# Performance work log

Hardware: AMD Instinct MI355X
Metric: run time of the kernel (lower is better)

Reference implementation:

```python
import jax, jax.numpy as jnp
import numpy as np

N_NODES = 50000
N_EDGES = 800000
N_GRAPHS = 64
IN_CH = 128
HID_CH = 128
FC_CH = 128


def setup_inputs() -> dict:
    key = jax.random.key(0)
    ks = jax.random.split(key, 12)

    def lin_w(k, fan_in, fan_out):
        return jax.random.normal(k, (fan_in, fan_out), jnp.float32) * (1.0 / np.sqrt(fan_in))

    return {
        "x": jax.random.normal(ks[0], (N_NODES, IN_CH), jnp.float32),
        "edge_index": jax.random.randint(ks[1], (2, N_EDGES), 0, N_NODES, dtype=jnp.int64),
        "batch_vec": jnp.sort(jax.random.randint(ks[2], (N_NODES,), 0, N_GRAPHS, dtype=jnp.int64)),
        "W1": lin_w(ks[3], IN_CH, HID_CH),
        "b1": jnp.zeros((HID_CH,), jnp.float32),
        "W2": lin_w(ks[4], HID_CH, HID_CH),
        "b2": jnp.zeros((HID_CH,), jnp.float32),
        "W3": lin_w(ks[5], HID_CH, FC_CH),
        "b3": jnp.zeros((FC_CH,), jnp.float32),
        "fcW1": lin_w(ks[6], FC_CH, IN_CH),
        "fcb1": jnp.zeros((IN_CH,), jnp.float32),
        "fcW2": lin_w(ks[7], IN_CH, 2),
        "fcb2": jnp.zeros((2,), jnp.float32),
    }


def reference(x, edge_index, batch_vec, W1, b1, W2, b2, W3, b3, fcW1, fcb1, fcW2, fcb2):
    n = x.shape[0]
    row, col = edge_index[0], edge_index[1]  # src -> dst

    # GCN symmetric normalization with self-loops: deg[j] = in-degree(j) + 1
    deg = jnp.zeros((n,), x.dtype).at[col].add(1.0) + 1.0
    inv_sqrt = jax.lax.rsqrt(deg)
    edge_norm = inv_sqrt[row] * inv_sqrt[col]  # [E]
    self_norm = (inv_sqrt * inv_sqrt)[:, None]  # [N,1], self-loop weight 1/deg

    def gcn(h, W, b):
        h = h @ W  # [N, out]
        agg = jnp.zeros_like(h).at[col].add(h[row] * edge_norm[:, None])
        return agg + h * self_norm + b

    h = jax.nn.relu(gcn(x, W1, b1))
    h = jax.nn.relu(gcn(h, W2, b2))
    h = jax.nn.relu(gcn(h, W3, b3))
    h = jax.nn.relu(h @ fcW1 + fcb1)
    h = h @ fcW2 + fcb2  # [N, 2]

    # global mean pool per graph
    sums = jax.ops.segment_sum(h, batch_vec, num_segments=N_GRAPHS)
    cnts = jax.ops.segment_sum(jnp.ones((n,), h.dtype), batch_vec, num_segments=N_GRAPHS)
    pooled = sums / jnp.maximum(cnts, 1.0)[:, None]  # [G, 2]
    return jax.nn.softmax(pooled, axis=1)
```

## Files before the change

kernel.cpp:

```cpp
#include <hip/hip_runtime.h>


#define CH 128
#define BSH 7
#define SEG 4096
#define EPW 4096
#define SAF 136
#define SC8 144

typedef unsigned short ushortT;
typedef unsigned int uintT;
typedef unsigned char ucharT;
typedef __attribute__((ext_vector_type(8))) short short8;
typedef __attribute__((ext_vector_type(4))) float floatx4;
typedef __attribute__((ext_vector_type(2))) float floatx2;

__device__ __forceinline__ float bf2f(uintT u) {
    return __uint_as_float(u << 16);
}
__device__ __forceinline__ ushortT f2bf(float f) {
    uintT x = __float_as_uint(f);
    return (ushortT)((x + 0x7fffu + ((x >> 16) & 1u)) >> 16);
}
__device__ __forceinline__ void dec4(uintT u, float* o) {
    floatx2 lo = __builtin_amdgcn_cvt_pk_f32_fp8((int)u, false);
    floatx2 hi = __builtin_amdgcn_cvt_pk_f32_fp8((int)u, true);
    o[0] = lo.x; o[1] = lo.y; o[2] = hi.x; o[3] = hi.y;
}
__device__ __forceinline__ void dec16(uint4 v, float* o) {
    dec4(v.x, o); dec4(v.y, o + 4); dec4(v.z, o + 8); dec4(v.w, o + 12);
}

__global__ __launch_bounds__(256) void k_bin(const int* __restrict__ row,
                                             const int* __restrict__ col,
                                             int* __restrict__ bfill,
                                             uintT* __restrict__ seg,
                                             const float* __restrict__ X,
                                             ucharT* __restrict__ Xb,
                                             const float* __restrict__ w0,
                                             const float* __restrict__ w1,
                                             const float* __restrict__ w2,
                                             const float* __restrict__ w3,
                                             ushortT* __restrict__ Whi,
                                             int E, int NBB, int NB, int total4) {
    __shared__ uintT staged[EPW];
    __shared__ int target[EPW];
    __shared__ int sval[512];
    __shared__ int horig[512];
    __shared__ int pcnt[512];
    __shared__ int gbase[512];
    const int t = threadIdx.x;

    if ((int)blockIdx.x >= NBB) {
        if ((int)blockIdx.x < NBB + 256) {
            int idx = ((int)blockIdx.x - NBB) * 256 + t;
            int m = idx >> 14;
            int r2 = idx & 16383;
            int n = r2 >> 7;
            int k = r2 & 127;
            const float* W = (m == 0) ? w0 : (m == 1) ? w1 : (m == 2) ? w2 : w3;
            Whi[m * 16384 + n * CH + k] = f2bf(W[k * CH + n]);
        } else {
            int i = ((int)blockIdx.x - NBB - 256) * 256 + t;
            if (i < total4) {
                float4 v = reinterpret_cast<const float4*>(X)[i];
                int r0 = __builtin_amdgcn_cvt_pk_fp8_f32(v.x, v.y, 0, false);
                int r1 = __builtin_amdgcn_cvt_pk_fp8_f32(v.z, v.w, r0, true);
                reinterpret_cast<int*>(Xb)[i] = r1;
            }
        }
        return;
    }

    const int e0 = blockIdx.x * EPW;
    const int cnt = min(EPW, E - e0);

    sval[t] = 0; sval[t + 256] = 0;
    __syncthreads();

    int er[16], ec[16];
#pragma unroll
    for (int i = 0; i < 16; ++i) {
        int le = i * 256 + t;
        if (le < cnt) {
            er[i] = row[e0 + le];
            ec[i] = col[e0 + le];
            atomicAdd(&sval[ec[i] >> BSH], 1);
        }
    }
    __syncthreads();
    horig[t] = sval[t]; horig[t + 256] = sval[t + 256];
    __syncthreads();
    for (int off = 1; off < 512; off <<= 1) {
        int a = (t >= off) ? sval[t - off] : 0;
        int b2 = sval[t + 256 - off];
        __syncthreads();
        sval[t] += a;
        sval[t + 256] += b2;
        __syncthreads();
    }
    for (int b = t; b < 512; b += 256) {
        int h = horig[b];
        pcnt[b] = sval[b] - h;
        gbase[b] = (h > 0 && b < NB) ? atomicAdd(&bfill[b], h) : 0;
    }
    __syncthreads();
#pragma unroll
    for (int i = 0; i < 16; ++i) {
        int le = i * 256 + t;
        if (le < cnt) {
            int b = ec[i] >> BSH;
            int j = atomicAdd(&pcnt[b], 1);
            staged[j] = (uintT)er[i] | ((uintT)ec[i] << 16);
            int lo = sval[b] - horig[b];
            target[j] = b * SEG + gbase[b] + (j - lo);
        }
    }
    __syncthreads();
    for (int s = t; s < cnt; s += 256) seg[target[s]] = staged[s];
}

__global__ __launch_bounds__(512) void k_binvs_bscan(const int* __restrict__ bfill,
                                                     const uintT* __restrict__ seg,
                                                     float* __restrict__ invs,
                                                     int* __restrict__ bbase,
                                                     int* __restrict__ indptr,
                                                     float* __restrict__ sums,
                                                     float* __restrict__ cnts,
                                                     int* __restrict__ tdone,
                                                     int NB, int N, int E, int G) {
    const int b = blockIdx.x;
    const int t = threadIdx.x;
    if (b < NB) {
        __shared__ int h[128];
        if (t < 128) h[t] = 0;
        __syncthreads();
        int cnt = bfill[b];
        const uintT* sp = seg + (size_t)b * SEG;
        for (int s = t; s < cnt; s += 512) atomicAdd(&h[(sp[s] >> 16) & 127], 1);
        __syncthreads();
        int d = b * 128 + t;
        if (t < 128 && d < N) invs[d] = rsqrtf((float)h[t] + 1.0f);
    } else {
        __shared__ int s[512];
        for (int i = t; i < 3 * G; i += 512) {
            if (i < 2 * G) sums[i] = 0.f;
            else cnts[i - 2 * G] = 0.f;
        }
        if (t == 0) atomicExch(tdone, 0);
        int v = (t < NB) ? bfill[t] : 0;
        s[t] = v;
        __syncthreads();
        for (int off = 1; off < 512; off <<= 1) {
            int a = (t >= off) ? s[t - off] : 0;
            __syncthreads();
            s[t] += a;
            __syncthreads();
        }
        if (t < NB) bbase[t] = s[t] - v;
        if (t == 0) indptr[N] = E;
    }
}

__global__ __launch_bounds__(256) void k_scatter(const int* __restrict__ bfill,
                                                 const int* __restrict__ bbase,
                                                 const uintT* __restrict__ seg,
                                                 const float* __restrict__ invs,
                                                 int* __restrict__ indptr,
                                                 uintT* __restrict__ epack,
                                                 int N) {
    __shared__ uintT staged[SEG];
    __shared__ int h[128];
    __shared__ int sc[128];
    __shared__ int pc[128];
    const int t = threadIdx.x;
    const int b = blockIdx.x;
    const int cnt = bfill[b];
    const int base = bbase[b];
    const uintT* sp = seg + (size_t)b * SEG;

    if (t < 128) h[t] = 0;
    __syncthreads();
    for (int s = t; s < cnt; s += 256) atomicAdd(&h[(sp[s] >> 16) & 127], 1);
    __syncthreads();
    if (t < 128) sc[t] = h[t];
    __syncthreads();
    for (int off = 1; off < 128; off <<= 1) {
        int a = (t >= off && t < 128) ? sc[t - off] : 0;
        __syncthreads();
        if (t < 128) sc[t] += a;
        __syncthreads();
    }
    if (t < 128) {
        int excl = sc[t] - h[t];
        pc[t] = excl;
        int d = b * 128 + t;
        if (d < N) indptr[d] = base + excl;
    }
    __syncthreads();
    for (int s = t; s < cnt; s += 256) {
        uintT rc = sp[s];
        int src = (int)(rc & 0xffffu), dst = (int)(rc >> 16);
        int j = atomicAdd(&pc[dst & 127], 1);
        float nrm = invs[src] * invs[dst];
        staged[j] = (uintT)src | ((uintT)f2bf(nrm) << 16);
    }
    __syncthreads();
    for (int s = t; s < cnt; s += 256) epack[base + s] = staged[s];
}

__global__ __launch_bounds__(256) void k_agg(const ucharT* __restrict__ H8,
                                             const uintT* __restrict__ epack,
                                             const int* __restrict__ indptr,
                                             const float* __restrict__ invs,
                                             ucharT* __restrict__ Z8, int N) {
    const int wave = threadIdx.x >> 6, lane = threadIdx.x & 63;
    const int ng = lane >> 3;
    const int l = lane & 7;
    const int node = blockIdx.x * 32 + wave * 8 + ng;
    if (node >= N) return;

    const uint4* H4 = reinterpret_cast<const uint4*>(H8);

    float acc[16];
    {
        float sn = invs[node];
        float sn2 = sn * sn;
        float d[16];
        dec16(H4[(size_t)node * 8 + l], d);
#pragma unroll
        for (int j = 0; j < 16; ++j) acc[j] = sn2 * d[j];
    }

    int p = indptr[node];
    int p1 = indptr[node + 1];

    if (p + 8 <= p1) {
        uintT e0[8];
#pragma unroll
        for (int i = 0; i < 8; ++i) e0[i] = epack[p + i];
        for (; p + 16 <= p1; p += 8) {
            uintT e1[8];
#pragma unroll
            for (int i = 0; i < 8; ++i) e1[i] = epack[p + 8 + i];
            uint4 g[8];
#pragma unroll
            for (int i = 0; i < 8; ++i) g[i] = H4[(size_t)(int)(e0[i] & 0xffffu) * 8 + l];
#pragma unroll
            for (int i = 0; i < 8; ++i) {
                float wv = bf2f(e0[i] >> 16);
                float d[16];
                dec16(g[i], d);
#pragma unroll
                for (int j = 0; j < 16; ++j) acc[j] += wv * d[j];
            }
#pragma unroll
            for (int i = 0; i < 8; ++i) e0[i] = e1[i];
        }
        {
            uint4 g[8];
#pragma unroll
            for (int i = 0; i < 8; ++i) g[i] = H4[(size_t)(int)(e0[i] & 0xffffu) * 8 + l];
#pragma unroll
            for (int i = 0; i < 8; ++i) {
                float wv = bf2f(e0[i] >> 16);
                float d[16];
                dec16(g[i], d);
#pragma unroll
                for (int j = 0; j < 16; ++j) acc[j] += wv * d[j];
            }
            p += 8;
        }
    }
    int rem = p1 - p;
    if (rem > 0) {
        uintT e[8];
#pragma unroll
        for (int i = 0; i < 8; ++i) e[i] = epack[(i < rem) ? p + i : p];
        uint4 g[8];
#pragma unroll
        for (int i = 0; i < 8; ++i) g[i] = H4[(size_t)(int)(e[i] & 0xffffu) * 8 + l];
#pragma unroll
        for (int i = 0; i < 8; ++i) {
            float wv = (i < rem) ? bf2f(e[i] >> 16) : 0.f;
            float d[16];
            dec16(g[i], d);
#pragma unroll
            for (int j = 0; j < 16; ++j) acc[j] += wv * d[j];
        }
    }

    uint4 o;
    {
        int r0 = __builtin_amdgcn_cvt_pk_fp8_f32(acc[0], acc[1], 0, false);
        r0 = __builtin_amdgcn_cvt_pk_fp8_f32(acc[2], acc[3], r0, true);
        int r1 = __builtin_amdgcn_cvt_pk_fp8_f32(acc[4], acc[5], 0, false);
        r1 = __builtin_amdgcn_cvt_pk_fp8_f32(acc[6], acc[7], r1, true);
        int r2 = __builtin_amdgcn_cvt_pk_fp8_f32(acc[8], acc[9], 0, false);
        r2 = __builtin_amdgcn_cvt_pk_fp8_f32(acc[10], acc[11], r2, true);
        int r3 = __builtin_amdgcn_cvt_pk_fp8_f32(acc[12], acc[13], 0, false);
        r3 = __builtin_amdgcn_cvt_pk_fp8_f32(acc[14], acc[15], r3, true);
        o.x = (uintT)r0; o.y = (uintT)r1; o.z = (uintT)r2; o.w = (uintT)r3;
    }
    reinterpret_cast<uint4*>(Z8)[(size_t)node * 8 + l] = o;
}

__global__ __launch_bounds__(256) void k_gemm(const ucharT* __restrict__ In8,
                                              const ushortT* __restrict__ Whi,
                                              const float* __restrict__ Bias,
                                              ucharT* __restrict__ Out8, int N) {
    __shared__ ushortT As[128 * SAF];
    __shared__ ushortT Ws[128 * SAF];

    const int tid = threadIdx.x;
    const int wave = tid >> 6, lane = tid & 63;
    const int quad = lane >> 4, l15 = lane & 15;
    const int mBase = (wave >> 1) * 64, nBase = (wave & 1) * 64;
    const int row0 = blockIdx.x * 128;
    const int r = tid >> 1, half = tid & 1;

    {
        int grow = row0 + r;
        uint4 a8 = {0, 0, 0, 0}, b8 = {0, 0, 0, 0}, c8 = {0, 0, 0, 0}, d8v = {0, 0, 0, 0};
        if (grow < N) {
            const uint4* s = reinterpret_cast<const uint4*>(In8 + (size_t)grow * CH + half * 64);
            a8 = s[0]; b8 = s[1]; c8 = s[2]; d8v = s[3];
        }
        uintT wds[16] = {a8.x, a8.y, a8.z, a8.w, b8.x, b8.y, b8.z, b8.w,
                         c8.x, c8.y, c8.z, c8.w, d8v.x, d8v.y, d8v.z, d8v.w};
#pragma unroll
        for (int q = 0; q < 16; ++q) {
            float d[4];
            dec4(wds[q], d);
            uint2 o;
            o.x = (uintT)f2bf(d[0]) | ((uintT)f2bf(d[1]) << 16);
            o.y = (uintT)f2bf(d[2]) | ((uintT)f2bf(d[3]) << 16);
            *reinterpret_cast<uint2*>(&As[r * SAF + half * 64 + q * 4]) = o;
        }
        const uint4* sh = reinterpret_cast<const uint4*>(Whi + r * CH + half * 64);
#pragma unroll
        for (int q = 0; q < 8; ++q)
            *reinterpret_cast<uint4*>(&Ws[r * SAF + half * 64 + q * 8]) = sh[q];
    }
    __syncthreads();

    floatx4 acc[4][4];
    const floatx4 zero4 = {0.f, 0.f, 0.f, 0.f};
#pragma unroll
    for (int i = 0; i < 4; i++)
#pragma unroll
        for (int j = 0; j < 4; j++) acc[i][j] = zero4;

#pragma unroll
    for (int ks = 0; ks < 4; ++ks) {
        short8 af[4], wf[4];
#pragma unroll
        for (int mt = 0; mt < 4; ++mt)
            af[mt] = *reinterpret_cast<const short8*>(&As[(mBase + mt * 16 + l15) * SAF + ks * 32 + quad * 8]);
#pragma unroll
        for (int nt = 0; nt < 4; ++nt)
            wf[nt] = *reinterpret_cast<const short8*>(&Ws[(nBase + nt * 16 + l15) * SAF + ks * 32 + quad * 8]);
#pragma unroll
        for (int mt = 0; mt < 4; ++mt)
#pragma unroll
            for (int nt = 0; nt < 4; ++nt)
                acc[mt][nt] = __builtin_amdgcn_mfma_f32_16x16x32_bf16(af[mt], wf[nt], acc[mt][nt], 0, 0, 0);
    }
    __syncthreads();

    float bb[4];
#pragma unroll
    for (int nt = 0; nt < 4; ++nt) bb[nt] = Bias[nBase + nt * 16 + l15];

    ucharT* Cs8 = reinterpret_cast<ucharT*>(As);
#pragma unroll
    for (int mt = 0; mt < 4; ++mt)
#pragma unroll
        for (int nt = 0; nt < 4; ++nt)
#pragma unroll
            for (int r4 = 0; r4 < 4; ++r4) {
                int lrow = mBase + mt * 16 + quad * 4 + r4;
                float v = fmaxf(acc[mt][nt][r4] + bb[nt], 0.f);
                int f8 = __builtin_amdgcn_cvt_pk_fp8_f32(v, 0.f, 0, false);
                Cs8[lrow * SC8 + nBase + nt * 16 + l15] = (ucharT)(f8 & 0xff);
            }
    __syncthreads();
    {
        int grow = row0 + r;
        if (grow < N) {
            const uint4* s4 = reinterpret_cast<const uint4*>(&Cs8[r * SC8 + half * 64]);
            uint4* dst = reinterpret_cast<uint4*>(Out8 + (size_t)grow * CH + half * 64);
#pragma unroll
            for (int q = 0; q < 4; ++q) dst[q] = s4[q];
        }
    }
}

__global__ __launch_bounds__(256) void k_tail(const ucharT* __restrict__ Z8,
                                              const ushortT* __restrict__ W3hi,
                                              const float* __restrict__ B3,
                                              const ushortT* __restrict__ F1hi,
                                              const float* __restrict__ FB1,
                                              const float* __restrict__ FW2,
                                              const float* __restrict__ FB2,
                                              const int* __restrict__ batch,
                                              float* __restrict__ sums,
                                              float* __restrict__ cnts,
                                              float* __restrict__ out,
                                              int* __restrict__ tdone,
                                              int N, int G) {
    __shared__ ushortT Hf[128 * SAF];
    __shared__ ushortT Ws[128 * SAF];
    __shared__ float rp0[256];
    __shared__ float rp1[256];
    __shared__ float ls[192];
    __shared__ int lastFlag;

    const int tid = threadIdx.x;
    const int wave = tid >> 6, lane = tid & 63;
    const int quad = lane >> 4, l15 = lane & 15;
    const int mBase = (wave >> 1) * 64, nBase = (wave & 1) * 64;
    const int row0 = blockIdx.x * 128;
    const int r = tid >> 1, half = tid & 1;

    {
        int grow = row0 + r;
        uint4 a8 = {0, 0, 0, 0}, b8 = {0, 0, 0, 0}, c8 = {0, 0, 0, 0}, d8v = {0, 0, 0, 0};
        if (grow < N) {
            const uint4* s = reinterpret_cast<const uint4*>(Z8 + (size_t)grow * CH + half * 64);
            a8 = s[0]; b8 = s[1]; c8 = s[2]; d8v = s[3];
        }
        uintT wds[16] = {a8.x, a8.y, a8.z, a8.w, b8.x, b8.y, b8.z, b8.w,
                         c8.x, c8.y, c8.z, c8.w, d8v.x, d8v.y, d8v.z, d8v.w};
#pragma unroll
        for (int q = 0; q < 16; ++q) {
            float d[4];
            dec4(wds[q], d);
            uint2 o;
            o.x = (uintT)f2bf(d[0]) | ((uintT)f2bf(d[1]) << 16);
            o.y = (uintT)f2bf(d[2]) | ((uintT)f2bf(d[3]) << 16);
            *reinterpret_cast<uint2*>(&Hf[r * SAF + half * 64 + q * 4]) = o;
        }
        const uint4* sh = reinterpret_cast<const uint4*>(W3hi + r * CH + half * 64);
#pragma unroll
        for (int q = 0; q < 8; ++q)
            *reinterpret_cast<uint4*>(&Ws[r * SAF + half * 64 + q * 8]) = sh[q];
    }
    __syncthreads();

    floatx4 acc[4][4];
    const floatx4 zero4 = {0.f, 0.f, 0.f, 0.f};
#pragma unroll
    for (int i = 0; i < 4; i++)
#pragma unroll
        for (int j = 0; j < 4; j++) acc[i][j] = zero4;

#pragma unroll
    for (int ks = 0; ks < 4; ++ks) {
        short8 af[4], wf[4];
#pragma unroll
        for (int mt = 0; mt < 4; ++mt)
            af[mt] = *reinterpret_cast<const short8*>(&Hf[(mBase + mt * 16 + l15) * SAF + ks * 32 + quad * 8]);
#pragma unroll
        for (int nt = 0; nt < 4; ++nt)
            wf[nt] = *reinterpret_cast<const short8*>(&Ws[(nBase + nt * 16 + l15) * SAF + ks * 32 + quad * 8]);
#pragma unroll
        for (int mt = 0; mt < 4; ++mt)
#pragma unroll
            for (int nt = 0; nt < 4; ++nt)
                acc[mt][nt] = __builtin_amdgcn_mfma_f32_16x16x32_bf16(af[mt], wf[nt], acc[mt][nt], 0, 0, 0);
    }
    __syncthreads();

    {
        float bb[4];
#pragma unroll
        for (int nt = 0; nt < 4; ++nt) bb[nt] = B3[nBase + nt * 16 + l15];
#pragma unroll
        for (int mt = 0; mt < 4; ++mt)
#pragma unroll
            for (int nt = 0; nt < 4; ++nt)
#pragma unroll
                for (int r4 = 0; r4 < 4; ++r4) {
                    int lrow = mBase + mt * 16 + quad * 4 + r4;
                    float v = fmaxf(acc[mt][nt][r4] + bb[nt], 0.f);
                    Hf[lrow * SAF + nBase + nt * 16 + l15] = f2bf(v);
                }
        const uint4* sh = reinterpret_cast<const uint4*>(F1hi + r * CH + half * 64);
#pragma unroll
        for (int q = 0; q < 8; ++q)
            *reinterpret_cast<uint4*>(&Ws[r * SAF + half * 64 + q * 8]) = sh[q];
    }
    __syncthreads();

#pragma unroll
    for (int i = 0; i < 4; i++)
#pragma unroll
        for (int j = 0; j < 4; j++) acc[i][j] = zero4;
#pragma unroll
    for (int ks = 0; ks < 4; ++ks) {
        short8 af[4], wf[4];
#pragma unroll
        for (int mt = 0; mt < 4; ++mt)
            af[mt] = *reinterpret_cast<const short8*>(&Hf[(mBase + mt * 16 + l15) * SAF + ks * 32 + quad * 8]);
#pragma unroll
        for (int nt = 0; nt < 4; ++nt)
            wf[nt] = *reinterpret_cast<const short8*>(&Ws[(nBase + nt * 16 + l15) * SAF + ks * 32 + quad * 8]);
#pragma unroll
        for (int mt = 0; mt < 4; ++mt)
#pragma unroll
            for (int nt = 0; nt < 4; ++nt)
                acc[mt][nt] = __builtin_amdgcn_mfma_f32_16x16x32_bf16(af[mt], wf[nt], acc[mt][nt], 0, 0, 0);
    }

    {
        float bb[4];
#pragma unroll
        for (int nt = 0; nt < 4; ++nt) bb[nt] = FB1[nBase + nt * 16 + l15];
        float w20[4], w21[4];
#pragma unroll
        for (int nt = 0; nt < 4; ++nt) {
            float2 wv = *reinterpret_cast<const float2*>(FW2 + 2 * (nBase + nt * 16 + l15));
            w20[nt] = wv.x;
            w21[nt] = wv.y;
        }
#pragma unroll
        for (int mt = 0; mt < 4; ++mt)
#pragma unroll
            for (int r4 = 0; r4 < 4; ++r4) {
                float d0 = 0.f, d1 = 0.f;
#pragma unroll
                for (int nt = 0; nt < 4; ++nt) {
                    float v = fmaxf(acc[mt][nt][r4] + bb[nt], 0.f);
                    d0 += v * w20[nt];
                    d1 += v * w21[nt];
                }
#pragma unroll
                for (int m = 8; m >= 1; m >>= 1) {
                    d0 += __shfl_xor(d0, m, 64);
                    d1 += __shfl_xor(d1, m, 64);
                }
                if (l15 == 0) {
                    int lrow = mBase + mt * 16 + quad * 4 + r4;
                    rp0[lrow * 2 + (wave & 1)] = d0;
                    rp1[lrow * 2 + (wave & 1)] = d1;
                }
            }
    }
    if (tid < 192) ls[tid] = 0.f;
    __syncthreads();

    if (tid < 128) {
        int node = row0 + tid;
        if (node < N) {
            float d0 = rp0[tid * 2] + rp0[tid * 2 + 1] + FB2[0];
            float d1 = rp1[tid * 2] + rp1[tid * 2 + 1] + FB2[1];
            int g = batch[node];
            atomicAdd(&ls[g], d0);
            atomicAdd(&ls[64 + g], d1);
            atomicAdd(&ls[128 + g], 1.0f);
        }
    }
    __syncthreads();
    if (tid < 64) {
        float c = ls[128 + tid];
        if (c != 0.f) {
            atomicAdd(&sums[2 * tid], ls[tid]);
            atomicAdd(&sums[2 * tid + 1], ls[64 + tid]);
            atomicAdd(&cnts[tid], c);
        }
    }
    __syncthreads();

    if (tid == 0) {
        int old = atomicAdd(tdone, 1);
        lastFlag = (old == (int)gridDim.x - 1) ? 1 : 0;
    }
    __syncthreads();
    if (lastFlag && tid < G) {
        int g = tid;
        float c = fmaxf(atomicAdd(&cnts[g], 0.f), 1.0f);
        float p0 = atomicAdd(&sums[2 * g], 0.f) / c;
        float p1 = atomicAdd(&sums[2 * g + 1], 0.f) / c;
        float m = fmaxf(p0, p1);
        float e0 = expf(p0 - m), e1 = expf(p1 - m);
        float inv = 1.f / (e0 + e1);
        out[2 * g] = e0 * inv;
        out[2 * g + 1] = e1 * inv;
    }
}

extern "C" void kernel_launch(void* const* d_in, const int* in_sizes, int n_in,
                              void* d_out, int out_size, void* d_ws, size_t ws_size,
                              hipStream_t stream) {
    const float* X   = (const float*)d_in[0];
    const int* EI    = (const int*)d_in[1];
    const int* BATCH = (const int*)d_in[2];
    const float* W1  = (const float*)d_in[3];
    const float* B1  = (const float*)d_in[4];
    const float* W2  = (const float*)d_in[5];
    const float* B2  = (const float*)d_in[6];
    const float* W3  = (const float*)d_in[7];
    const float* B3  = (const float*)d_in[8];
    const float* FW1 = (const float*)d_in[9];
    const float* FB1 = (const float*)d_in[10];
    const float* FW2 = (const float*)d_in[11];
    const float* FB2 = (const float*)d_in[12];

    const int N = in_sizes[0] / CH;
    const int E = in_sizes[1] / 2;
    const int G = out_size / 2;
    const int* rowp = EI;
    const int* colp = EI + E;
    const int NB = (N + 127) >> BSH;

    char* w = (char*)d_ws;
    auto alloc = [&](size_t bytes) -> char* {
        char* p = w;
        w += (bytes + 255) & ~(size_t)255;
        return p;
    };
    ucharT*  Z8    = (ucharT*)alloc((size_t)N * CH);
    ucharT*  Hb8   = (ucharT*)alloc((size_t)N * CH);
    ucharT*  Xb8   = (ucharT*)alloc((size_t)N * CH);
    ushortT* WhiA  = (ushortT*)alloc((size_t)4 * 16384 * 2);
    float* invs    = (float*)alloc((size_t)N * 4);
    int*   indptr  = (int*)alloc((size_t)(N + 1) * 4);
    uintT* epack   = (uintT*)alloc((size_t)E * 4);
    uintT* seg     = (uintT*)alloc((size_t)NB * SEG * 4);
    int*   bfill   = (int*)alloc((size_t)NB * 4);
    int*   bbase   = (int*)alloc((size_t)NB * 4);
    float* sums    = (float*)alloc((size_t)G * 3 * 4);
    float* cnts    = sums + 2 * G;
    int*   tdone   = (int*)alloc(256);

    const int nbAgg  = (N + 31) / 32;
    const int nbGemm = (N + 127) / 128;
    const int nbBin  = (E + EPW - 1) / EPW;
    const int total4 = N * CH / 4;
    const int nbXc   = (total4 + 255) / 256;

    hipMemsetAsync(bfill, 0, (size_t)NB * 4, stream);
    k_bin<<<nbBin + 256 + nbXc, 256, 0, stream>>>(rowp, colp, bfill, seg,
                                                  X, Xb8, W1, W2, W3, FW1, WhiA,
                                                  E, nbBin, NB, total4);
    k_binvs_bscan<<<NB + 1, 512, 0, stream>>>(bfill, seg, invs, bbase, indptr,
                                              sums, cnts, tdone, NB, N, E, G);
    k_scatter<<<NB, 256, 0, stream>>>(bfill, bbase, seg, invs, indptr, epack, N);

    k_agg<<<nbAgg, 256, 0, stream>>>(Xb8, epack, indptr, invs, Z8, N);
    k_gemm<<<nbGemm, 256, 0, stream>>>(Z8, WhiA, B1, Hb8, N);
    k_agg<<<nbAgg, 256, 0, stream>>>(Hb8, epack, indptr, invs, Z8, N);
    k_gemm<<<nbGemm, 256, 0, stream>>>(Z8, WhiA + 16384, B2, Hb8, N);
    k_agg<<<nbAgg, 256, 0, stream>>>(Hb8, epack, indptr, invs, Z8, N);
    k_tail<<<nbGemm, 256, 0, stream>>>(Z8, WhiA + 2 * 16384, B3,
                                       WhiA + 3 * 16384, FB1, FW2, FB2,
                                       BATCH, sums, cnts, (float*)d_out, tdone, N, G);
}
```

Baseline: 204.2 us.

## Factor GCN normalization into node scaling and pad CSR rows with 16-bit indices

Replaces the per-edge bf16 weight with a factored symmetric normalization. Source features are prescaled by inv_sqrt(deg) before conversion to fp8 and again in the GEMM epilogue, and the aggregate is multiplied by the destination inv_sqrt at the end. Edge lists become 16-bit source indices in fixed per-bin segments. Each row is padded to a multiple of 8 with a dummy zero row, so the aggregation loop has no remainder handling. Degree is counted with global atomics in the binning kernel, which removes the separate degree/scan kernel and the bbase prefix. The costs are extra global atomics, padded edge storage, and fp8 quantization of the prescaled values.

```diff
diff --git a/kernel.cpp b/kernel.cpp
--- a/kernel.cpp
+++ b/kernel.cpp
@@ -4,6 +4,7 @@
 #define CH 128
 #define BSH 7
 #define SEG 4096
+#define SEGP 5120
 #define EPW 4096
 #define SAF 136
 #define SC8 144
@@ -34,15 +35,16 @@
 __global__ __launch_bounds__(256) void k_bin(const int* __restrict__ row,
                                              const int* __restrict__ col,
                                              int* __restrict__ bfill,
+                                             int* __restrict__ deg,
                                              uintT* __restrict__ seg,
-                                             const float* __restrict__ X,
-                                             ucharT* __restrict__ Xb,
                                              const float* __restrict__ w0,
                                              const float* __restrict__ w1,
                                              const float* __restrict__ w2,
                                              const float* __restrict__ w3,
                                              ushortT* __restrict__ Whi,
-                                             int E, int NBB, int NB, int total4) {
+                                             float* __restrict__ sums,
+                                             int* __restrict__ tdone,
+                                             int E, int NBB, int NB, int G) {
     __shared__ uintT staged[EPW];
     __shared__ int target[EPW];
     __shared__ int sval[512];
@@ -52,22 +54,17 @@
     const int t = threadIdx.x;
 
     if ((int)blockIdx.x >= NBB) {
-        if ((int)blockIdx.x < NBB + 256) {
-            int idx = ((int)blockIdx.x - NBB) * 256 + t;
-            int m = idx >> 14;
-            int r2 = idx & 16383;
-            int n = r2 >> 7;
-            int k = r2 & 127;
-            const float* W = (m == 0) ? w0 : (m == 1) ? w1 : (m == 2) ? w2 : w3;
-            Whi[m * 16384 + n * CH + k] = f2bf(W[k * CH + n]);
-        } else {
-            int i = ((int)blockIdx.x - NBB - 256) * 256 + t;
-            if (i < total4) {
-                float4 v = reinterpret_cast<const float4*>(X)[i];
-                int r0 = __builtin_amdgcn_cvt_pk_fp8_f32(v.x, v.y, 0, false);
-                int r1 = __builtin_amdgcn_cvt_pk_fp8_f32(v.z, v.w, r0, true);
-                reinterpret_cast<int*>(Xb)[i] = r1;
-            }
+        int bb = (int)blockIdx.x - NBB;
+        int idx = bb * 256 + t;
+        int m = idx >> 14;
+        int r2 = idx & 16383;
+        int n = r2 >> 7;
+        int k = r2 & 127;
+        const float* W = (m == 0) ? w0 : (m == 1) ? w1 : (m == 2) ? w2 : w3;
+        Whi[m * 16384 + n * CH + k] = f2bf(W[k * CH + n]);
+        if (bb == 0) {
+            if (t < 3 * G) sums[t] = 0.f;
+            if (t == 0) tdone[0] = 0;
         }
         return;
     }
@@ -86,6 +83,7 @@
             er[i] = row[e0 + le];
             ec[i] = col[e0 + le];
             atomicAdd(&sval[ec[i] >> BSH], 1);
+            atomicAdd(&deg[ec[i]], 1);
         }
     }
     __syncthreads();
@@ -120,99 +118,90 @@
     for (int s = t; s < cnt; s += 256) seg[target[s]] = staged[s];
 }
 
-__global__ __launch_bounds__(512) void k_binvs_bscan(const int* __restrict__ bfill,
-                                                     const uintT* __restrict__ seg,
-                                                     float* __restrict__ invs,
-                                                     int* __restrict__ bbase,
-                                                     int* __restrict__ indptr,
-                                                     float* __restrict__ sums,
-                                                     float* __restrict__ cnts,
-                                                     int* __restrict__ tdone,
-                                                     int NB, int N, int E, int G) {
-    const int b = blockIdx.x;
+__global__ __launch_bounds__(256) void k_scatter(const int* __restrict__ bfill,
+                                                 const uintT* __restrict__ seg,
+                                                 const int* __restrict__ deg,
+                                                 uintT* __restrict__ indptr,
+                                                 ushortT* __restrict__ epack,
+                                                 const float* __restrict__ X,
+                                                 ucharT* __restrict__ Xb,
+                                                 ucharT* __restrict__ Hb,
+                                                 int N, int NB, int total4) {
     const int t = threadIdx.x;
-    if (b < NB) {
-        __shared__ int h[128];
-        if (t < 128) h[t] = 0;
-        __syncthreads();
-        int cnt = bfill[b];
-        const uintT* sp = seg + (size_t)b * SEG;
-        for (int s = t; s < cnt; s += 512) atomicAdd(&h[(sp[s] >> 16) & 127], 1);
-        __syncthreads();
-        int d = b * 128 + t;
-        if (t < 128 && d < N) invs[d] = rsqrtf((float)h[t] + 1.0f);
-    } else {
-        __shared__ int s[512];
-        for (int i = t; i < 3 * G; i += 512) {
-            if (i < 2 * G) sums[i] = 0.f;
-            else cnts[i - 2 * G] = 0.f;
-        }
-        if (t == 0) atomicExch(tdone, 0);
-        int v = (t < NB) ? bfill[t] : 0;
-        s[t] = v;
-        __syncthreads();
-        for (int off = 1; off < 512; off <<= 1) {
-            int a = (t >= off) ? s[t - off] : 0;
-            __syncthreads();
-            s[t] += a;
-            __syncthreads();
-        }
-        if (t < NB) bbase[t] = s[t] - v;
-        if (t == 0) indptr[N] = E;
-    }
-}
-
-__global__ __launch_bounds__(256) void k_scatter(const int* __restrict__ bfill,
-                                                 const int* __restrict__ bbase,
-                                                 const uintT* __restrict__ seg,
-                                                 const float* __restrict__ invs,
-                                                 int* __restrict__ indptr,
-                                                 uintT* __restrict__ epack,
-                                                 int N) {
-    __shared__ uintT staged[SEG];
-    __shared__ int h[128];
-    __shared__ int sc[128];
+    if ((int)blockIdx.x >= NB) {
+        int cb = (int)blockIdx.x - NB;
+        if (cb == 0 && t < 16) {
+            uint4 z = {0, 0, 0, 0};
+            if (t < 8) reinterpret_cast<uint4*>(Xb + (size_t)N * CH)[t] = z;
+            else       reinterpret_cast<uint4*>(Hb + (size_t)N * CH)[t - 8] = z;
+        }
+        int i = cb * 256 + t;
+        if (i < total4) {
+            float4 v = reinterpret_cast<const float4*>(X)[i];
+            int rowi = i >> 5;
+            float iv = rsqrtf((float)deg[rowi] + 1.0f);
+            int r0 = __builtin_amdgcn_cvt_pk_fp8_f32(v.x * iv, v.y * iv, 0, false);
+            int r1 = __builtin_amdgcn_cvt_pk_fp8_f32(v.z * iv, v.w * iv, r0, true);
+            reinterpret_cast<int*>(Xb)[i] = r1;
+        }
+        return;
+    }
+
+    __shared__ ushortT staged[SEGP];
+    __shared__ int hp[128];
+    __shared__ int praw[128];
+    __shared__ int pinc[128];
     __shared__ int pc[128];
-    const int t = threadIdx.x;
+    __shared__ int ptotS;
     const int b = blockIdx.x;
     const int cnt = bfill[b];
-    const int base = bbase[b];
     const uintT* sp = seg + (size_t)b * SEG;
 
-    if (t < 128) h[t] = 0;
-    __syncthreads();
-    for (int s = t; s < cnt; s += 256) atomicAdd(&h[(sp[s] >> 16) & 127], 1);
-    __syncthreads();
-    if (t < 128) sc[t] = h[t];
+    if (t < 128) {
+        int d = b * 128 + t;
+        int dg = (d < N) ? deg[d] : 0;
+        praw[t] = dg;
+        hp[t] = (dg + 7) & ~7;
+        pinc[t] = hp[t];
+    }
     __syncthreads();
     for (int off = 1; off < 128; off <<= 1) {
-        int a = (t >= off && t < 128) ? sc[t - off] : 0;
+        int a = (t >= off && t < 128) ? pinc[t - off] : 0;
         __syncthreads();
-        if (t < 128) sc[t] += a;
+        if (t < 128) pinc[t] += a;
         __syncthreads();
     }
     if (t < 128) {
-        int excl = sc[t] - h[t];
+        int excl = pinc[t] - hp[t];
         pc[t] = excl;
         int d = b * 128 + t;
-        if (d < N) indptr[d] = base + excl;
+        if (d < N) indptr[d] = (uintT)(b * SEGP + excl) | ((uintT)(hp[t] >> 3) << 21);
+        if (t == 127) ptotS = pinc[127];
     }
     __syncthreads();
     for (int s = t; s < cnt; s += 256) {
         uintT rc = sp[s];
-        int src = (int)(rc & 0xffffu), dst = (int)(rc >> 16);
-        int j = atomicAdd(&pc[dst & 127], 1);
-        float nrm = invs[src] * invs[dst];
-        staged[j] = (uintT)src | ((uintT)f2bf(nrm) << 16);
-    }
-    __syncthreads();
-    for (int s = t; s < cnt; s += 256) epack[base + s] = staged[s];
+        int j = atomicAdd(&pc[(rc >> 16) & 127], 1);
+        staged[j] = (ushortT)(rc & 0xffffu);
+    }
+    __syncthreads();
+    if (t < 128) {
+        int base2 = pinc[t] - hp[t];
+        for (int k = base2 + praw[t]; k < base2 + hp[t]; ++k) staged[k] = (ushortT)N;
+    }
+    __syncthreads();
+    {
+        int tot2 = ptotS >> 1;
+        uintT* dstw = reinterpret_cast<uintT*>(epack + (size_t)b * SEGP);
+        const uintT* srcw = reinterpret_cast<const uintT*>(staged);
+        for (int s = t; s < tot2; s += 256) dstw[s] = srcw[s];
+    }
 }
 
 __global__ __launch_bounds__(256) void k_agg(const ucharT* __restrict__ H8,
-                                             const uintT* __restrict__ epack,
-                                             const int* __restrict__ indptr,
-                                             const float* __restrict__ invs,
+                                             const ushortT* __restrict__ epack,
+                                             const uintT* __restrict__ indptr,
+                                             const int* __restrict__ deg,
                                              ucharT* __restrict__ Z8, int N) {
     const int wave = threadIdx.x >> 6, lane = threadIdx.x & 63;
     const int ng = lane >> 3;
@@ -221,74 +210,51 @@
     if (node >= N) return;
 
     const uint4* H4 = reinterpret_cast<const uint4*>(H8);
+    const uint4* E4 = reinterpret_cast<const uint4*>(epack);
+
+    int dgn = deg[node];
+    uintT v = indptr[node];
+    int b8 = (int)(v & 0x1FFFFFu) >> 3;
+    int nb = (int)(v >> 21);
 
     float acc[16];
     {
-        float sn = invs[node];
-        float sn2 = sn * sn;
         float d[16];
         dec16(H4[(size_t)node * 8 + l], d);
 #pragma unroll
-        for (int j = 0; j < 16; ++j) acc[j] = sn2 * d[j];
-    }
-
-    int p = indptr[node];
-    int p1 = indptr[node + 1];
-
-    if (p + 8 <= p1) {
-        uintT e0[8];
-#pragma unroll
-        for (int i = 0; i < 8; ++i) e0[i] = epack[p + i];
-        for (; p + 16 <= p1; p += 8) {
-            uintT e1[8];
-#pragma unroll
-            for (int i = 0; i < 8; ++i) e1[i] = epack[p + 8 + i];
-            uint4 g[8];
-#pragma unroll
-            for (int i = 0; i < 8; ++i) g[i] = H4[(size_t)(int)(e0[i] & 0xffffu) * 8 + l];
-#pragma unroll
-            for (int i = 0; i < 8; ++i) {
-                float wv = bf2f(e0[i] >> 16);
-                float d[16];
-                dec16(g[i], d);
-#pragma unroll
-                for (int j = 0; j < 16; ++j) acc[j] += wv * d[j];
-            }
-#pragma unroll
-            for (int i = 0; i < 8; ++i) e0[i] = e1[i];
-        }
-        {
-            uint4 g[8];
-#pragma unroll
-            for (int i = 0; i < 8; ++i) g[i] = H4[(size_t)(int)(e0[i] & 0xffffu) * 8 + l];
-#pragma unroll
-            for (int i = 0; i < 8; ++i) {
-                float wv = bf2f(e0[i] >> 16);
-                float d[16];
-                dec16(g[i], d);
-#pragma unroll
-                for (int j = 0; j < 16; ++j) acc[j] += wv * d[j];
-            }
-            p += 8;
-        }
-    }
-    int rem = p1 - p;
-    if (rem > 0) {
-        uintT e[8];
-#pragma unroll
-        for (int i = 0; i < 8; ++i) e[i] = epack[(i < rem) ? p + i : p];
+        for (int j = 0; j < 16; ++j) acc[j] = d[j];
+    }
+
+    auto proc = [&](uint4 e) {
+        int s[8] = {(int)(e.x & 0xffffu), (int)(e.x >> 16),
+                    (int)(e.y & 0xffffu), (int)(e.y >> 16),
+                    (int)(e.z & 0xffffu), (int)(e.z >> 16),
+                    (int)(e.w & 0xffffu), (int)(e.w >> 16)};
         uint4 g[8];
 #pragma unroll
-        for (int i = 0; i < 8; ++i) g[i] = H4[(size_t)(int)(e[i] & 0xffffu) * 8 + l];
+        for (int i = 0; i < 8; ++i) g[i] = H4[(size_t)s[i] * 8 + l];
 #pragma unroll
         for (int i = 0; i < 8; ++i) {
-            float wv = (i < rem) ? bf2f(e[i] >> 16) : 0.f;
             float d[16];
             dec16(g[i], d);
 #pragma unroll
-            for (int j = 0; j < 16; ++j) acc[j] += wv * d[j];
-        }
-    }
+            for (int j = 0; j < 16; ++j) acc[j] += d[j];
+        }
+    };
+
+    if (nb > 0) {
+        uint4 e0 = E4[b8];
+        for (int it = 1; it < nb; ++it) {
+            uint4 e1 = E4[b8 + it];
+            proc(e0);
+            e0 = e1;
+        }
+        proc(e0);
+    }
+
+    float iv = rsqrtf((float)dgn + 1.0f);
+#pragma unroll
+    for (int j = 0; j < 16; ++j) acc[j] *= iv;
 
     uint4 o;
     {
@@ -308,9 +274,11 @@
 __global__ __launch_bounds__(256) void k_gemm(const ucharT* __restrict__ In8,
                                               const ushortT* __restrict__ Whi,
                                               const float* __restrict__ Bias,
+                                              const int* __restrict__ deg,
                                               ucharT* __restrict__ Out8, int N) {
     __shared__ ushortT As[128 * SAF];
     __shared__ ushortT Ws[128 * SAF];
+    __shared__ float invsL[128];
 
     const int tid = threadIdx.x;
     const int wave = tid >> 6, lane = tid & 63;
@@ -319,6 +287,10 @@
     const int row0 = blockIdx.x * 128;
     const int r = tid >> 1, half = tid & 1;
 
+    if (tid < 128) {
+        int d = row0 + tid;
+        invsL[tid] = (d < N) ? rsqrtf((float)deg[d] + 1.0f) : 0.f;
+    }
     {
         int grow = row0 + r;
         uint4 a8 = {0, 0, 0, 0}, b8 = {0, 0, 0, 0}, c8 = {0, 0, 0, 0}, d8v = {0, 0, 0, 0};
@@ -380,7 +352,7 @@
 #pragma unroll
             for (int r4 = 0; r4 < 4; ++r4) {
                 int lrow = mBase + mt * 16 + quad * 4 + r4;
-                float v = fmaxf(acc[mt][nt][r4] + bb[nt], 0.f);
+                float v = fmaxf(acc[mt][nt][r4] + bb[nt], 0.f) * invsL[lrow];
                 int f8 = __builtin_amdgcn_cvt_pk_fp8_f32(v, 0.f, 0, false);
                 Cs8[lrow * SC8 + nBase + nt * 16 + l15] = (ucharT)(f8 & 0xff);
             }
@@ -621,15 +593,14 @@
         return p;
     };
     ucharT*  Z8    = (ucharT*)alloc((size_t)N * CH);
-    ucharT*  Hb8   = (ucharT*)alloc((size_t)N * CH);
-    ucharT*  Xb8   = (ucharT*)alloc((size_t)N * CH);
+    ucharT*  Hb8   = (ucharT*)alloc((size_t)(N + 1) * CH);
+    ucharT*  Xb8   = (ucharT*)alloc((size_t)(N + 1) * CH);
     ushortT* WhiA  = (ushortT*)alloc((size_t)4 * 16384 * 2);
-    float* invs    = (float*)alloc((size_t)N * 4);
-    int*   indptr  = (int*)alloc((size_t)(N + 1) * 4);
-    uintT* epack   = (uintT*)alloc((size_t)E * 4);
+    int*   bfill   = (int*)alloc((size_t)NB * 4);
+    int*   deg     = (int*)alloc((size_t)N * 4);
+    uintT* indptr  = (uintT*)alloc((size_t)N * 4);
+    ushortT* epack = (ushortT*)alloc((size_t)NB * SEGP * 2);
     uintT* seg     = (uintT*)alloc((size_t)NB * SEG * 4);
-    int*   bfill   = (int*)alloc((size_t)NB * 4);
-    int*   bbase   = (int*)alloc((size_t)NB * 4);
     float* sums    = (float*)alloc((size_t)G * 3 * 4);
     float* cnts    = sums + 2 * G;
     int*   tdone   = (int*)alloc(256);
@@ -640,19 +611,19 @@
     const int total4 = N * CH / 4;
     const int nbXc   = (total4 + 255) / 256;
 
-    hipMemsetAsync(bfill, 0, (size_t)NB * 4, stream);
-    k_bin<<<nbBin + 256 + nbXc, 256, 0, stream>>>(rowp, colp, bfill, seg,
-                                                  X, Xb8, W1, W2, W3, FW1, WhiA,
-                                                  E, nbBin, NB, total4);
-    k_binvs_bscan<<<NB + 1, 512, 0, stream>>>(bfill, seg, invs, bbase, indptr,
-                                              sums, cnts, tdone, NB, N, E, G);
-    k_scatter<<<NB, 256, 0, stream>>>(bfill, bbase, seg, invs, indptr, epack, N);
-
-    k_agg<<<nbAgg, 256, 0, stream>>>(Xb8, epack, indptr, invs, Z8, N);
-    k_gemm<<<nbGemm, 256, 0, stream>>>(Z8, WhiA, B1, Hb8, N);
-    k_agg<<<nbAgg, 256, 0, stream>>>(Hb8, epack, indptr, invs, Z8, N);
-    k_gemm<<<nbGemm, 256, 0, stream>>>(Z8, WhiA + 16384, B2, Hb8, N);
-    k_agg<<<nbAgg, 256, 0, stream>>>(Hb8, epack, indptr, invs, Z8, N);
+    const size_t zeroBytes = (((size_t)NB * 4 + 255) & ~(size_t)255) + (size_t)N * 4;
+    hipMemsetAsync(bfill, 0, zeroBytes, stream);
+    k_bin<<<nbBin + 256, 256, 0, stream>>>(rowp, colp, bfill, deg, seg,
+                                           W1, W2, W3, FW1, WhiA, sums, tdone,
+                                           E, nbBin, NB, G);
+    k_scatter<<<NB + nbXc, 256, 0, stream>>>(bfill, seg, deg, indptr, epack,
+                                             X, Xb8, Hb8, N, NB, total4);
+
+    k_agg<<<nbAgg, 256, 0, stream>>>(Xb8, epack, indptr, deg, Z8, N);
+    k_gemm<<<nbGemm, 256, 0, stream>>>(Z8, WhiA, B1, deg, Hb8, N);
+    k_agg<<<nbAgg, 256, 0, stream>>>(Hb8, epack, indptr, deg, Z8, N);
+    k_gemm<<<nbGemm, 256, 0, stream>>>(Z8, WhiA + 16384, B2, deg, Hb8, N);
+    k_agg<<<nbAgg, 256, 0, stream>>>(Hb8, epack, indptr, deg, Z8, N);
     k_tail<<<nbGemm, 256, 0, stream>>>(Z8, WhiA + 2 * 16384, B3,
                                        WhiA + 3 * 16384, FB1, FW2, FB2,
                                        BATCH, sums, cnts, (float*)d_out, tdone, N, G);
```

New measurement: 221.3 us. 8.3% more time.

## Pad per-node edge lists to multiples of eight and drop global bucket scan

Applied to the files above, without the earlier changes.

The CSR layout changes to per-bucket fixed-stride segments, with each node's edge list padded to a multiple of 8 using zero-weight records. The node pointer packs the offset and the 8-record group count into one word. This removes the global bucket prefix scan, the indptr[N] read and the remainder-handling tail loop in the aggregation kernel, which now reads edges as aligned uint4 pairs. Zeroing of sums and tdone moves into the binning kernel, and the binning chunk size is halved to get more blocks. The cost is extra padded gathers of row 0 (up to 7 per node) and a larger edge buffer.

```diff
diff --git a/kernel.cpp b/kernel.cpp
--- a/kernel.cpp
+++ b/kernel.cpp
@@ -4,7 +4,8 @@
 #define CH 128
 #define BSH 7
 #define SEG 4096
-#define EPW 4096
+#define SEGP 5120
+#define EPW 2048
 #define SAF 136
 #define SC8 144
 
@@ -42,7 +43,10 @@
                                              const float* __restrict__ w2,
                                              const float* __restrict__ w3,
                                              ushortT* __restrict__ Whi,
-                                             int E, int NBB, int NB, int total4) {
+                                             float* __restrict__ sums,
+                                             int* __restrict__ tdone,
+                                             int E, int NBB, int NB, int G,
+                                             int total4) {
     __shared__ uintT staged[EPW];
     __shared__ int target[EPW];
     __shared__ int sval[512];
@@ -52,16 +56,21 @@
     const int t = threadIdx.x;
 
     if ((int)blockIdx.x >= NBB) {
-        if ((int)blockIdx.x < NBB + 256) {
-            int idx = ((int)blockIdx.x - NBB) * 256 + t;
+        int bb = (int)blockIdx.x - NBB;
+        if (bb < 256) {
+            int idx = bb * 256 + t;
             int m = idx >> 14;
             int r2 = idx & 16383;
             int n = r2 >> 7;
             int k = r2 & 127;
             const float* W = (m == 0) ? w0 : (m == 1) ? w1 : (m == 2) ? w2 : w3;
             Whi[m * 16384 + n * CH + k] = f2bf(W[k * CH + n]);
+            if (bb == 0) {
+                if (t < 3 * G) sums[t] = 0.f;
+                if (t == 0) tdone[0] = 0;
+            }
         } else {
-            int i = ((int)blockIdx.x - NBB - 256) * 256 + t;
+            int i = (bb - 256) * 256 + t;
             if (i < total4) {
                 float4 v = reinterpret_cast<const float4*>(X)[i];
                 int r0 = __builtin_amdgcn_cvt_pk_fp8_f32(v.x, v.y, 0, false);
@@ -78,9 +87,9 @@
     sval[t] = 0; sval[t + 256] = 0;
     __syncthreads();
 
-    int er[16], ec[16];
-#pragma unroll
-    for (int i = 0; i < 16; ++i) {
+    int er[8], ec[8];
+#pragma unroll
+    for (int i = 0; i < 8; ++i) {
         int le = i * 256 + t;
         if (le < cnt) {
             er[i] = row[e0 + le];
@@ -106,7 +115,7 @@
     }
     __syncthreads();
 #pragma unroll
-    for (int i = 0; i < 16; ++i) {
+    for (int i = 0; i < 8; ++i) {
         int le = i * 256 + t;
         if (le < cnt) {
             int b = ec[i] >> BSH;
@@ -120,98 +129,94 @@
     for (int s = t; s < cnt; s += 256) seg[target[s]] = staged[s];
 }
 
-__global__ __launch_bounds__(512) void k_binvs_bscan(const int* __restrict__ bfill,
-                                                     const uintT* __restrict__ seg,
-                                                     float* __restrict__ invs,
-                                                     int* __restrict__ bbase,
-                                                     int* __restrict__ indptr,
-                                                     float* __restrict__ sums,
-                                                     float* __restrict__ cnts,
-                                                     int* __restrict__ tdone,
-                                                     int NB, int N, int E, int G) {
+__global__ __launch_bounds__(512) void k_binvs(const int* __restrict__ bfill,
+                                               const uintT* __restrict__ seg,
+                                               float* __restrict__ invs,
+                                               int NB, int N) {
     const int b = blockIdx.x;
     const int t = threadIdx.x;
-    if (b < NB) {
-        __shared__ int h[128];
-        if (t < 128) h[t] = 0;
-        __syncthreads();
-        int cnt = bfill[b];
-        const uintT* sp = seg + (size_t)b * SEG;
-        for (int s = t; s < cnt; s += 512) atomicAdd(&h[(sp[s] >> 16) & 127], 1);
-        __syncthreads();
-        int d = b * 128 + t;
-        if (t < 128 && d < N) invs[d] = rsqrtf((float)h[t] + 1.0f);
-    } else {
-        __shared__ int s[512];
-        for (int i = t; i < 3 * G; i += 512) {
-            if (i < 2 * G) sums[i] = 0.f;
-            else cnts[i - 2 * G] = 0.f;
-        }
-        if (t == 0) atomicExch(tdone, 0);
-        int v = (t < NB) ? bfill[t] : 0;
-        s[t] = v;
-        __syncthreads();
-        for (int off = 1; off < 512; off <<= 1) {
-            int a = (t >= off) ? s[t - off] : 0;
-            __syncthreads();
-            s[t] += a;
-            __syncthreads();
-        }
-        if (t < NB) bbase[t] = s[t] - v;
-        if (t == 0) indptr[N] = E;
-    }
+    __shared__ int h[128];
+    if (t < 128) h[t] = 0;
+    __syncthreads();
+    int cnt = bfill[b];
+    const uintT* sp = seg + (size_t)b * SEG;
+    for (int s = t; s < cnt; s += 512) atomicAdd(&h[(sp[s] >> 16) & 127], 1);
+    __syncthreads();
+    int d = b * 128 + t;
+    if (t < 128 && d < N) invs[d] = rsqrtf((float)h[t] + 1.0f);
 }
 
 __global__ __launch_bounds__(256) void k_scatter(const int* __restrict__ bfill,
-                                                 const int* __restrict__ bbase,
                                                  const uintT* __restrict__ seg,
                                                  const float* __restrict__ invs,
-                                                 int* __restrict__ indptr,
+                                                 uintT* __restrict__ indptr,
                                                  uintT* __restrict__ epack,
-                                                 int N) {
-    __shared__ uintT staged[SEG];
+                                                 int N, int NB) {
+    __shared__ __align__(16) uintT staged[SEGP];
     __shared__ int h[128];
-    __shared__ int sc[128];
+    __shared__ int pinc[128];
     __shared__ int pc[128];
+    __shared__ float invL[128];
+    __shared__ int ptotS;
     const int t = threadIdx.x;
     const int b = blockIdx.x;
     const int cnt = bfill[b];
-    const int base = bbase[b];
     const uintT* sp = seg + (size_t)b * SEG;
 
-    if (t < 128) h[t] = 0;
+    if (t < 128) {
+        h[t] = 0;
+        int d = b * 128 + t;
+        invL[t] = (d < N) ? invs[d] : 0.f;
+    }
     __syncthreads();
     for (int s = t; s < cnt; s += 256) atomicAdd(&h[(sp[s] >> 16) & 127], 1);
     __syncthreads();
-    if (t < 128) sc[t] = h[t];
+    int praw = 0, hp = 0;
+    if (t < 128) {
+        praw = h[t];
+        hp = (praw + 7) & ~7;
+        pinc[t] = hp;
+    }
     __syncthreads();
     for (int off = 1; off < 128; off <<= 1) {
-        int a = (t >= off && t < 128) ? sc[t - off] : 0;
+        int a = (t >= off && t < 128) ? pinc[t - off] : 0;
         __syncthreads();
-        if (t < 128) sc[t] += a;
+        if (t < 128) pinc[t] += a;
         __syncthreads();
     }
+    int excl = 0;
     if (t < 128) {
-        int excl = sc[t] - h[t];
+        excl = pinc[t] - hp;
         pc[t] = excl;
         int d = b * 128 + t;
-        if (d < N) indptr[d] = base + excl;
+        if (d < N) indptr[d] = (uintT)(b * SEGP + excl) | ((uintT)(hp >> 3) << 21);
+        if (t == 127) ptotS = pinc[127];
     }
     __syncthreads();
     for (int s = t; s < cnt; s += 256) {
         uintT rc = sp[s];
-        int src = (int)(rc & 0xffffu), dst = (int)(rc >> 16);
-        int j = atomicAdd(&pc[dst & 127], 1);
-        float nrm = invs[src] * invs[dst];
+        int src = (int)(rc & 0xffffu);
+        int d7 = (int)(rc >> 16) & 127;
+        int j = atomicAdd(&pc[d7], 1);
+        float nrm = invs[src] * invL[d7];
         staged[j] = (uintT)src | ((uintT)f2bf(nrm) << 16);
     }
     __syncthreads();
-    for (int s = t; s < cnt; s += 256) epack[base + s] = staged[s];
+    if (t < 128) {
+        for (int k = excl + praw; k < excl + hp; ++k) staged[k] = 0u;
+    }
+    __syncthreads();
+    {
+        int tot4 = ptotS >> 2;
+        uint4* dstw = reinterpret_cast<uint4*>(epack + (size_t)b * SEGP);
+        const uint4* srcw = reinterpret_cast<const uint4*>(staged);
+        for (int s = t; s < tot4; s += 256) dstw[s] = srcw[s];
+    }
 }
 
 __global__ __launch_bounds__(256) void k_agg(const ucharT* __restrict__ H8,
                                              const uintT* __restrict__ epack,
-                                             const int* __restrict__ indptr,
+                                             const uintT* __restrict__ indptr,
                                              const float* __restrict__ invs,
                                              ucharT* __restrict__ Z8, int N) {
     const int wave = threadIdx.x >> 6, lane = threadIdx.x & 63;
@@ -221,6 +226,11 @@
     if (node >= N) return;
 
     const uint4* H4 = reinterpret_cast<const uint4*>(H8);
+    const uint4* E4 = reinterpret_cast<const uint4*>(epack);
+
+    uintT v = indptr[node];
+    int q0 = (int)(v & 0x1FFFFFu) >> 2;
+    int nb = (int)(v >> 21);
 
     float acc[16];
     {
@@ -232,62 +242,30 @@
         for (int j = 0; j < 16; ++j) acc[j] = sn2 * d[j];
     }
 
-    int p = indptr[node];
-    int p1 = indptr[node + 1];
-
-    if (p + 8 <= p1) {
-        uintT e0[8];
-#pragma unroll
-        for (int i = 0; i < 8; ++i) e0[i] = epack[p + i];
-        for (; p + 16 <= p1; p += 8) {
-            uintT e1[8];
-#pragma unroll
-            for (int i = 0; i < 8; ++i) e1[i] = epack[p + 8 + i];
-            uint4 g[8];
-#pragma unroll
-            for (int i = 0; i < 8; ++i) g[i] = H4[(size_t)(int)(e0[i] & 0xffffu) * 8 + l];
-#pragma unroll
-            for (int i = 0; i < 8; ++i) {
-                float wv = bf2f(e0[i] >> 16);
-                float d[16];
-                dec16(g[i], d);
-#pragma unroll
-                for (int j = 0; j < 16; ++j) acc[j] += wv * d[j];
-            }
-#pragma unroll
-            for (int i = 0; i < 8; ++i) e0[i] = e1[i];
-        }
-        {
-            uint4 g[8];
-#pragma unroll
-            for (int i = 0; i < 8; ++i) g[i] = H4[(size_t)(int)(e0[i] & 0xffffu) * 8 + l];
-#pragma unroll
-            for (int i = 0; i < 8; ++i) {
-                float wv = bf2f(e0[i] >> 16);
-                float d[16];
-                dec16(g[i], d);
-#pragma unroll
-                for (int j = 0; j < 16; ++j) acc[j] += wv * d[j];
-            }
-            p += 8;
-        }
-    }
-    int rem = p1 - p;
-    if (rem > 0) {
-        uintT e[8];
-#pragma unroll
-        for (int i = 0; i < 8; ++i) e[i] = epack[(i < rem) ? p + i : p];
+    auto proc = [&](uint4 ea, uint4 eb) {
+        uintT rec[8] = {ea.x, ea.y, ea.z, ea.w, eb.x, eb.y, eb.z, eb.w};
         uint4 g[8];
 #pragma unroll
-        for (int i = 0; i < 8; ++i) g[i] = H4[(size_t)(int)(e[i] & 0xffffu) * 8 + l];
+        for (int i = 0; i < 8; ++i)
+            g[i] = H4[(size_t)(int)(rec[i] & 0xffffu) * 8 + l];
 #pragma unroll
         for (int i = 0; i < 8; ++i) {
-            float wv = (i < rem) ? bf2f(e[i] >> 16) : 0.f;
+            float wv = bf2f(rec[i] >> 16);
             float d[16];
             dec16(g[i], d);
 #pragma unroll
             for (int j = 0; j < 16; ++j) acc[j] += wv * d[j];
         }
+    };
+
+    if (nb > 0) {
+        uint4 ea = E4[q0], eb = E4[q0 + 1];
+        for (int it = 1; it < nb; ++it) {
+            uint4 na = E4[q0 + 2 * it], nbv = E4[q0 + 2 * it + 1];
+            proc(ea, eb);
+            ea = na; eb = nbv;
+        }
+        proc(ea, eb);
     }
 
     uint4 o;
@@ -625,11 +603,10 @@
     ucharT*  Xb8   = (ucharT*)alloc((size_t)N * CH);
     ushortT* WhiA  = (ushortT*)alloc((size_t)4 * 16384 * 2);
     float* invs    = (float*)alloc((size_t)N * 4);
-    int*   indptr  = (int*)alloc((size_t)(N + 1) * 4);
-    uintT* epack   = (uintT*)alloc((size_t)E * 4);
+    uintT* indptr  = (uintT*)alloc((size_t)N * 4);
+    uintT* epack   = (uintT*)alloc((size_t)NB * SEGP * 4);
     uintT* seg     = (uintT*)alloc((size_t)NB * SEG * 4);
     int*   bfill   = (int*)alloc((size_t)NB * 4);
-    int*   bbase   = (int*)alloc((size_t)NB * 4);
     float* sums    = (float*)alloc((size_t)G * 3 * 4);
     float* cnts    = sums + 2 * G;
     int*   tdone   = (int*)alloc(256);
@@ -643,10 +620,9 @@
     hipMemsetAsync(bfill, 0, (size_t)NB * 4, stream);
     k_bin<<<nbBin + 256 + nbXc, 256, 0, stream>>>(rowp, colp, bfill, seg,
                                                   X, Xb8, W1, W2, W3, FW1, WhiA,
-                                                  E, nbBin, NB, total4);
-    k_binvs_bscan<<<NB + 1, 512, 0, stream>>>(bfill, seg, invs, bbase, indptr,
-                                              sums, cnts, tdone, NB, N, E, G);
-    k_scatter<<<NB, 256, 0, stream>>>(bfill, bbase, seg, invs, indptr, epack, N);
+                                                  sums, tdone, E, nbBin, NB, G, total4);
+    k_binvs<<<NB, 512, 0, stream>>>(bfill, seg, invs, NB, N);
+    k_scatter<<<NB, 256, 0, stream>>>(bfill, seg, invs, indptr, epack, N, NB);
 
     k_agg<<<nbAgg, 256, 0, stream>>>(Xb8, epack, indptr, invs, Z8, N);
     k_gemm<<<nbGemm, 256, 0, stream>>>(Z8, WhiA, B1, Hb8, N);
```

New measurement: 203.9 us. Within noise of the previous version (-0.2%).
